# Kernel optimization log

Hardware: AMD Instinct MI355X
Metric: run time of the kernel (lower is better)

The kernel has to match this reference:

```python
import jax, jax.numpy as jnp
import numpy as np

TOP_K = 8
TEMPERATURE = 0.07
EPS = 1e-12  # matches torch F.normalize eps


def l2norm(x):
    return x / jnp.maximum(jnp.linalg.norm(x, axis=-1, keepdims=True), EPS)


def setup_inputs() -> dict:
    key = jax.random.key(0)
    k1, k2, k3, k4 = jax.random.split(key, 4)
    B, D, V, U, Q = 256, 768, 50257, 1000, 10000
    time_series_embedding = jax.random.normal(k1, (B, D), dtype=jnp.float32)
    word_embeddings = jax.random.normal(k2, (V, D), dtype=jnp.float32)
    # xavier_uniform-like init scale for the prototype parameter
    limit = float(np.sqrt(6.0 / (U + D)))
    tctp_embeddings = jax.random.uniform(k3, (U, D), dtype=jnp.float32, minval=-limit, maxval=limit)
    support_set = jax.random.normal(k4, (Q, D), dtype=jnp.float32)
    return {
        "time_series_embedding": time_series_embedding,
        "word_embeddings": word_embeddings,
        "tctp_embeddings": tctp_embeddings,
        "support_set": support_set,
    }


def reference(time_series_embedding, word_embeddings, tctp_embeddings, support_set):
    B = time_series_embedding.shape[0]

    # ---- L_proto: MSE between each word token and its nearest prototype ----
    # For unit vectors, cdist^2 = 2 - 2*cos_sim, so argmin(dist) == argmax(sim).
    w_norm = l2norm(word_embeddings)          # [V, D]
    t_norm = l2norm(tctp_embeddings)          # [U, D]
    sim_vu = jnp.einsum('vd,ud->vu', w_norm, t_norm)  # [V, U]
    nearest_idx = jnp.argmax(sim_vu, axis=1)          # [V]
    nearest_protos = t_norm[nearest_idx]              # [V, D]
    loss_proto = jnp.mean((w_norm - nearest_protos) ** 2)

    # ---- top-k nearest-neighbor TCTPs from the support set ----
    ts_norm = l2norm(time_series_embedding)   # [B, D]
    sup_norm = l2norm(support_set)            # [Q, D]
    sim_bq = jnp.einsum('bd,qd->bq', ts_norm, sup_norm)  # [B, Q]
    # smallest L2 distance == largest cosine similarity (unit vectors)
    _, topk_idx = jax.lax.top_k(sim_bq, TOP_K)           # [B, k]
    nearest_tctps = sup_norm[topk_idx]                   # [B, k, D]

    # ---- NNCL contrastive loss ----
    positive = l2norm(nearest_tctps.mean(axis=1))        # [B, D]
    pos_sim = jnp.sum(ts_norm * positive, axis=1) / TEMPERATURE   # [B]
    neg_sim = jnp.einsum('bd,cd->bc', ts_norm, ts_norm) / TEMPERATURE  # [B, B]
    neg_sim = jnp.where(jnp.eye(B, dtype=bool), -jnp.inf, neg_sim)
    logits = jnp.concatenate([pos_sim[:, None], neg_sim], axis=1)  # [B, 1+B]
    loss_nncl = -jnp.mean(jax.nn.log_softmax(logits, axis=1)[:, 0])

    return nearest_tctps, loss_proto, loss_nncl
```

## Files before the change

kernel.cpp:

```cpp
#include <hip/hip_runtime.h>
#include <hip/hip_bf16.h>
#include <math.h>

typedef __bf16 bf16_t;
typedef __bf16 bf16x8 __attribute__((ext_vector_type(8)));
typedef __bf16 bf16x4 __attribute__((ext_vector_type(4)));
typedef float  f32x4  __attribute__((ext_vector_type(4)));
typedef long   i64_t;
typedef unsigned long long u64_t;

#define D 768

__device__ inline double blk_sum(double x, double* s) {
#pragma unroll
  for (int m = 32; m; m >>= 1) x += __shfl_xor(x, m);
  __syncthreads();
  if ((threadIdx.x & 63) == 0) s[threadIdx.x >> 6] = x;
  __syncthreads();
  return s[0] + s[1] + s[2] + s[3];
}

__device__ inline double blk_max(double x, double* s) {
#pragma unroll
  for (int m = 32; m; m >>= 1) x = fmax(x, __shfl_xor(x, m));
  __syncthreads();
  if ((threadIdx.x & 63) == 0) s[threadIdx.x >> 6] = x;
  __syncthreads();
  return fmax(fmax(s[0], s[1]), fmax(s[2], s[3]));
}

__global__ __launch_bounds__(256) void norm_all(
    const float* __restrict__ Tm, const float* __restrict__ TS,
    const float* __restrict__ SUP, const float* __restrict__ Wm,
    u64_t* __restrict__ t8T, u64_t* __restrict__ w8t,
    float* __restrict__ wscale, float* __restrict__ ts_n,
    bf16_t* __restrict__ ts_bf, float* __restrict__ sup_n,
    double* __restrict__ accd,
    int U, int V, int B, int Q, int nbT, int nbTS, int nbSUP) {
  const int wave = threadIdx.x >> 6, lane = threadIdx.x & 63;
  const int bid = blockIdx.x;
  if (bid == 0 && threadIdx.x == 0) accd[0] = 0.0;

  if (bid < nbT) {
    const int row = bid * 4 + wave;
    double inv = 0.0;
    if (row < U) {
      const float4* s = (const float4*)(Tm + (size_t)row * D);
      double ss = 0.0;
#pragma unroll
      for (int j = 0; j < 3; j++) {
        float4 v = s[lane + 64 * j];
        ss += (double)v.x * v.x + (double)v.y * v.y +
              (double)v.z * v.z + (double)v.w * v.w;
      }
#pragma unroll
      for (int m = 32; m; m >>= 1) ss += __shfl_xor(ss, m);
      inv = 1.0 / fmax(sqrt(ss), 1e-12);
    }
    const float sc = (float)(inv * 16.0);
#pragma unroll
    for (int h = 0; h < 2; h++) {
      if (h == 1 && lane >= 32) continue;
      const int c = h * 64 + lane;
      u64_t frag = 0ull;
      if (row < U) {
        const float* p = Tm + (size_t)row * D + c * 8;
        float4 x = *(const float4*)p;
        float4 y = *(const float4*)(p + 4);
        int lo = __builtin_amdgcn_cvt_pk_fp8_f32(x.x * sc, x.y * sc, 0, false);
        lo = __builtin_amdgcn_cvt_pk_fp8_f32(x.z * sc, x.w * sc, lo, true);
        int hi = __builtin_amdgcn_cvt_pk_fp8_f32(y.x * sc, y.y * sc, 0, false);
        hi = __builtin_amdgcn_cvt_pk_fp8_f32(y.z * sc, y.w * sc, hi, true);
        frag = ((u64_t)(unsigned)hi << 32) | (unsigned)lo;
      }
      t8T[(size_t)c * 1024 + row] = frag;
    }
    return;
  }

  if (bid < nbT + nbTS + nbSUP) {
    const float* src;
    int row;
    bool is_ts = false;
    if (bid < nbT + nbTS) { row = (bid - nbT) * 4 + wave; src = TS; is_ts = true; }
    else                  { row = (bid - nbT - nbTS) * 4 + wave; src = SUP;
                            if (row >= Q) return; }
    const float4* s = (const float4*)(src + (size_t)row * D);
    float4 v[3];
    double ss = 0.0;
#pragma unroll
    for (int j = 0; j < 3; j++) {
      v[j] = s[lane + 64 * j];
      ss += (double)v[j].x * v[j].x + (double)v[j].y * v[j].y +
            (double)v[j].z * v[j].z + (double)v[j].w * v[j].w;
    }
#pragma unroll
    for (int m = 32; m; m >>= 1) ss += __shfl_xor(ss, m);
    double inv = 1.0 / fmax(sqrt(ss), 1e-12);
    float4 o[3];
#pragma unroll
    for (int j = 0; j < 3; j++) {
      o[j].x = (float)((double)v[j].x * inv);
      o[j].y = (float)((double)v[j].y * inv);
      o[j].z = (float)((double)v[j].z * inv);
      o[j].w = (float)((double)v[j].w * inv);
    }
    float* dst = is_ts ? ts_n : sup_n;
    float* drow = dst + (size_t)row * D;
#pragma unroll
    for (int j = 0; j < 3; j++) ((float4*)drow)[lane + 64 * j] = o[j];
    if (is_ts) {
      bf16_t* brow = ts_bf + (size_t)row * D;
#pragma unroll
      for (int j = 0; j < 3; j++) {
        bf16x4 ob;
        ob[0] = (bf16_t)o[j].x; ob[1] = (bf16_t)o[j].y;
        ob[2] = (bf16_t)o[j].z; ob[3] = (bf16_t)o[j].w;
        *(bf16x4*)(brow + 4 * (lane + 64 * j)) = ob;
      }
    }
    return;
  }

  {
    const int v0 = (bid - nbT - nbTS - nbSUP) * 64 + wave * 16;
    const int r  = lane & 15;
    const int cs = lane >> 4;
    const int v  = v0 + r;
    const bool valid = v < V;
    const float* Wp = Wm + (size_t)v * D;
    u64_t* tile = w8t + (size_t)(v0 >> 4) * 1536;
    float ssf = 0.f;
#pragma unroll
    for (int j = 0; j < 24; j++) {
      u64_t frag = 0ull;
      if (valid) {
        const float* p = Wp + (j * 4 + cs) * 8;
        float4 x = *(const float4*)p;
        float4 y = *(const float4*)(p + 4);
        ssf += x.x * x.x + x.y * x.y + x.z * x.z + x.w * x.w +
               y.x * y.x + y.y * y.y + y.z * y.z + y.w * y.w;
        int lo = __builtin_amdgcn_cvt_pk_fp8_f32(x.x * 16.f, x.y * 16.f, 0, false);
        lo = __builtin_amdgcn_cvt_pk_fp8_f32(x.z * 16.f, x.w * 16.f, lo, true);
        int hi = __builtin_amdgcn_cvt_pk_fp8_f32(y.x * 16.f, y.y * 16.f, 0, false);
        hi = __builtin_amdgcn_cvt_pk_fp8_f32(y.z * 16.f, y.w * 16.f, hi, true);
        frag = ((u64_t)(unsigned)hi << 32) | (unsigned)lo;
      }
      tile[j * 64 + lane] = frag;
    }
    ssf += __shfl_xor(ssf, 16);
    ssf += __shfl_xor(ssf, 32);
    if (cs == 0)
      wscale[v0 + r] = valid
          ? (float)(1.0 / (256.0 * fmax(sqrt((double)ssf), 1e-12)))
          : 0.f;
  }
}

__global__ __launch_bounds__(256) void maxsim_gemm(
    const u64_t* __restrict__ W8T, const u64_t* __restrict__ T8T,
    float* __restrict__ maxpart, int U, int vstride) {
  __shared__ u64_t bt[4 * 96 * 16];
  const int tid  = threadIdx.x;
  const int lane = tid & 63;
  const int r    = lane & 15;
  const int ks   = lane >> 4;
  const int g    = blockIdx.x;

  {
    const int pb = g * 64;
#pragma unroll
    for (int j = 0; j < 12; j++) {
      const int m = j * 256 + tid;
      const int s = m / 768;
      const int rem = m - s * 768;
      const int c = rem >> 3, h = rem & 7;
      ulonglong2 val = *(const ulonglong2*)(T8T + (size_t)c * 1024 + pb + s * 16 + h * 2);
      *(ulonglong2*)(bt + s * 1536 + c * 16 + h * 2) = val;
    }
  }
  __syncthreads();

  bool msk[4];
#pragma unroll
  for (int s = 0; s < 4; s++) msk[s] = (g * 64 + s * 16 + r) < U;

  const int wv = tid >> 6;
#pragma unroll
  for (int wt = 0; wt < 4; wt++) {
    const int v0 = blockIdx.y * 256 + wv * 64 + wt * 16;
    const u64_t* ap = W8T + (size_t)(v0 >> 4) * 1536;
    u64_t a[24];
#pragma unroll
    for (int kk = 0; kk < 24; kk++) a[kk] = ap[kk * 64 + lane];
    f32x4 ac0 = {0.f,0.f,0.f,0.f}, ac1 = {0.f,0.f,0.f,0.f};
    f32x4 ac2 = {0.f,0.f,0.f,0.f}, ac3 = {0.f,0.f,0.f,0.f};
#pragma unroll
    for (int kk = 0; kk < 24; kk++) {
      const int ci = kk * 64 + lane;
      ac0 = __builtin_amdgcn_mfma_f32_16x16x32_fp8_fp8(
          (i64_t)a[kk], (i64_t)bt[ci],            ac0, 0, 0, 0);
      ac1 = __builtin_amdgcn_mfma_f32_16x16x32_fp8_fp8(
          (i64_t)a[kk], (i64_t)bt[1536 + ci],     ac1, 0, 0, 0);
      ac2 = __builtin_amdgcn_mfma_f32_16x16x32_fp8_fp8(
          (i64_t)a[kk], (i64_t)bt[2 * 1536 + ci], ac2, 0, 0, 0);
      ac3 = __builtin_amdgcn_mfma_f32_16x16x32_fp8_fp8(
          (i64_t)a[kk], (i64_t)bt[3 * 1536 + ci], ac3, 0, 0, 0);
    }
    f32x4 mx = {-1e30f, -1e30f, -1e30f, -1e30f};
#pragma unroll
    for (int j = 0; j < 4; j++) {
      if (msk[0]) mx[j] = fmaxf(mx[j], ac0[j]);
      if (msk[1]) mx[j] = fmaxf(mx[j], ac1[j]);
      if (msk[2]) mx[j] = fmaxf(mx[j], ac2[j]);
      if (msk[3]) mx[j] = fmaxf(mx[j], ac3[j]);
    }
#pragma unroll
    for (int m = 1; m < 16; m <<= 1) {
#pragma unroll
      for (int j = 0; j < 4; j++) mx[j] = fmaxf(mx[j], __shfl_xor(mx[j], m));
    }
    if (r == 0) {
#pragma unroll
      for (int j = 0; j < 4; j++)
        maxpart[(size_t)g * vstride + v0 + ks * 4 + j] = mx[j];
    }
  }
}

#define LDSROW 776

__global__ __launch_bounds__(256) void simf_gemm(const float* __restrict__ SUPn,
                                                 const bf16_t* __restrict__ TSb,
                                                 float* __restrict__ sim,
                                                 int Q, int ld, int NTB) {
  __shared__ __align__(16) bf16_t lds[2][16 * LDSROW];
  const int tid  = threadIdx.x;
  const int lane = tid & 63;
  const int rowbase = blockIdx.x * 64 + (tid >> 6) * 16;
  const int arow_i  = rowbase + (lane & 15);

  bf16x8 a[24];
  if (arow_i < Q) {
    const float* ar = SUPn + (size_t)arow_i * D + ((lane >> 4) * 8);
#pragma unroll
    for (int kk = 0; kk < 24; kk++) {
      float4 x = *(const float4*)(ar + kk * 32);
      float4 y = *(const float4*)(ar + kk * 32 + 4);
      bf16x8 f;
      f[0] = (bf16_t)x.x; f[1] = (bf16_t)x.y; f[2] = (bf16_t)x.z; f[3] = (bf16_t)x.w;
      f[4] = (bf16_t)y.x; f[5] = (bf16_t)y.y; f[6] = (bf16_t)y.z; f[7] = (bf16_t)y.w;
      a[kk] = f;
    }
  } else {
#pragma unroll
    for (int kk = 0; kk < 24; kk++) {
      bf16x8 f;
#pragma unroll
      for (int e = 0; e < 8; e++) f[e] = (bf16_t)0.f;
      a[kk] = f;
    }
  }

  auto stage = [&](int buf, int nt) {
    const ulonglong2* src = (const ulonglong2*)(TSb + (size_t)nt * 16 * D);
#pragma unroll
    for (int j = 0; j < 6; j++) {
      int c = tid + j * 256;
      int rr = c / 96, w = c % 96;
      *(ulonglong2*)&lds[buf][rr * LDSROW + w * 8] = src[c];
    }
  };

  stage(0, 0);
  for (int nt = 0; nt < NTB; nt++) {
    __syncthreads();
    if (nt + 1 < NTB) stage((nt + 1) & 1, nt + 1);
    f32x4 acc = {0.f, 0.f, 0.f, 0.f};
    const bf16_t* brow = &lds[nt & 1][(lane & 15) * LDSROW + ((lane >> 4) * 8)];
#pragma unroll
    for (int kk = 0; kk < 24; kk++) {
      bf16x8 b = *(const bf16x8*)(brow + kk * 32);
      acc = __builtin_amdgcn_mfma_f32_16x16x32_bf16(a[kk], b, acc, 0, 0, 0);
    }
    const int bcol = nt * 16 + (lane & 15);
    const int q0   = rowbase + ((lane >> 4) << 2);
    float* dst = sim + (size_t)bcol * ld + q0;
    if (q0 + 3 < Q) {
      *(f32x4*)dst = acc;
    } else {
#pragma unroll
      for (int j = 0; j < 4; j++)
        if (q0 + j < Q) dst[j] = acc[j];
    }
  }
}

__global__ __launch_bounds__(256) void gram_gemm(const float* __restrict__ TSn,
                                                 float* __restrict__ gram, int Bn) {
  __shared__ float As[16][68];
  __shared__ float Bs[16][68];
  const int tid = threadIdx.x;
  const int tx = tid & 15, ty = tid >> 4;
  const int m0 = blockIdx.y * 64, n0 = blockIdx.x * 64;
  const int sr = tid >> 2, sk = (tid & 3) * 4;
  float acc[4][4] = {};
  for (int k0 = 0; k0 < D; k0 += 16) {
    __syncthreads();
    float4 av = *(const float4*)(TSn + (size_t)(m0 + sr) * D + k0 + sk);
    float4 bv = *(const float4*)(TSn + (size_t)(n0 + sr) * D + k0 + sk);
    As[sk + 0][sr] = av.x; As[sk + 1][sr] = av.y;
    As[sk + 2][sr] = av.z; As[sk + 3][sr] = av.w;
    Bs[sk + 0][sr] = bv.x; Bs[sk + 1][sr] = bv.y;
    Bs[sk + 2][sr] = bv.z; Bs[sk + 3][sr] = bv.w;
    __syncthreads();
#pragma unroll
    for (int k = 0; k < 16; k++) {
      float a0 = As[k][ty * 4 + 0], a1 = As[k][ty * 4 + 1];
      float a2 = As[k][ty * 4 + 2], a3 = As[k][ty * 4 + 3];
      float b0 = Bs[k][tx * 4 + 0], b1 = Bs[k][tx * 4 + 1];
      float b2 = Bs[k][tx * 4 + 2], b3 = Bs[k][tx * 4 + 3];
      acc[0][0] += a0 * b0; acc[0][1] += a0 * b1; acc[0][2] += a0 * b2; acc[0][3] += a0 * b3;
      acc[1][0] += a1 * b0; acc[1][1] += a1 * b1; acc[1][2] += a1 * b2; acc[1][3] += a1 * b3;
      acc[2][0] += a2 * b0; acc[2][1] += a2 * b1; acc[2][2] += a2 * b2; acc[2][3] += a2 * b3;
      acc[3][0] += a3 * b0; acc[3][1] += a3 * b1; acc[3][2] += a3 * b2; acc[3][3] += a3 * b3;
    }
  }
#pragma unroll
  for (int i = 0; i < 4; i++) {
    float4 o = {acc[i][0], acc[i][1], acc[i][2], acc[i][3]};
    *(float4*)(gram + (size_t)(m0 + ty * 4 + i) * Bn + n0 + tx * 4) = o;
  }
}

__device__ inline unsigned long long pack_key(float v, int q) {
  unsigned u = __float_as_uint(v);
  u = (u & 0x80000000u) ? ~u : (u | 0x80000000u);
  return ((unsigned long long)u << 32) | (unsigned)(0xFFFFFFFFu - (unsigned)q);
}

__global__ __launch_bounds__(256) void topk_nncl(const float* __restrict__ sim,
                                                 const float* __restrict__ gram,
                                                 const float* __restrict__ SUPn,
                                                 const float* __restrict__ TSn,
                                                 float* __restrict__ out,
                                                 double* __restrict__ row_loss,
                                                 int Q, int ld, int Bn) {
  __shared__ unsigned long long sk[256][16];
  __shared__ float tsrow[D];
  __shared__ double sval[16];
  __shared__ int    sidx[16];
  __shared__ double red[4];
  const int b = blockIdx.x, tid = threadIdx.x;
#pragma unroll
  for (int j = 0; j < 3; j++) tsrow[tid + 256 * j] = TSn[(size_t)b * D + tid + 256 * j];

  const float* row = sim + (size_t)b * ld;
  unsigned long long best[16];
#pragma unroll
  for (int k = 0; k < 16; k++) best[k] = 0ull;
  for (int q = tid; q < Q; q += 256) {
    unsigned long long key = pack_key(row[q], q);
    if (key > best[15]) {
      best[15] = key;
      for (int k = 15; k > 0; k--) {
        if (best[k] > best[k - 1]) {
          unsigned long long t = best[k]; best[k] = best[k - 1]; best[k - 1] = t;
        } else break;
      }
    }
  }
#pragma unroll
  for (int k = 0; k < 16; k++) sk[tid][k] = best[k];
  for (int stride = 128; stride >= 1; stride >>= 1) {
    __syncthreads();
    if (tid < stride) {
      unsigned long long outk[16];
      int pa = 0, pb = 0;
#pragma unroll
      for (int k = 0; k < 16; k++) {
        unsigned long long va = sk[tid][pa], vb = sk[tid + stride][pb];
        if (va >= vb) { outk[k] = va; pa++; }
        else          { outk[k] = vb; pb++; }
      }
#pragma unroll
      for (int k = 0; k < 16; k++) sk[tid][k] = outk[k];
    }
  }
  __syncthreads();

  const int lane = tid & 63, w = tid >> 6;
  for (int c = w; c < 16; c += 4) {
    int q = (int)(0xFFFFFFFFu - (unsigned)(sk[0][c] & 0xFFFFFFFFull));
    const float* sr = SUPn + (size_t)q * D;
    double dot = 0.0;
#pragma unroll
    for (int i = 0; i < 12; i++)
      dot += (double)sr[lane + 64 * i] * (double)tsrow[lane + 64 * i];
#pragma unroll
    for (int m = 32; m; m >>= 1) dot += __shfl_xor(dot, m);
    if (lane == 0) { sval[c] = dot; sidx[c] = q; }
  }
  __syncthreads();
  if (tid == 0) {
    for (int i = 1; i < 16; i++) {
      double v = sval[i]; int ix = sidx[i];
      int j = i - 1;
      while (j >= 0 && (sval[j] < v || (sval[j] == v && sidx[j] > ix))) {
        sval[j + 1] = sval[j]; sidx[j + 1] = sidx[j]; j--;
      }
      sval[j + 1] = v; sidx[j + 1] = ix;
    }
  }
  __syncthreads();

  float mean[3] = {0.f, 0.f, 0.f};
#pragma unroll
  for (int k = 0; k < 8; k++) {
    const float* sr = SUPn + (size_t)sidx[k] * D;
    float* orow = out + ((size_t)b * 8 + k) * D;
#pragma unroll
    for (int j = 0; j < 3; j++) {
      float x = sr[tid + 256 * j];
      orow[tid + 256 * j] = x;
      mean[j] += x;
    }
  }
#pragma unroll
  for (int j = 0; j < 3; j++) mean[j] *= 0.125f;
  double ss = 0.0;
#pragma unroll
  for (int j = 0; j < 3; j++) ss += (double)mean[j] * mean[j];
  ss = blk_sum(ss, red);
  double inv = 1.0 / fmax(sqrt(ss), 1e-12);
  double dot = 0.0;
#pragma unroll
  for (int j = 0; j < 3; j++)
    dot += (double)tsrow[tid + 256 * j] * ((double)mean[j] * inv);
  dot = blk_sum(dot, red);
  const double p = dot / (double)0.07f;

  const bool diag = (tid == b);
  double logit = (double)gram[(size_t)b * Bn + tid] / (double)0.07f;
  double m = blk_max(diag ? -1e300 : logit, red);
  m = fmax(m, p);
  double term = diag ? 0.0 : exp(logit - m);
  double ssum = blk_sum(term, red);
  ssum += exp(p - m);
  if (tid == 0) row_loss[b] = (log(ssum) + m) - p;
}

__global__ __launch_bounds__(256) void reduce_proto(
    const float* __restrict__ maxpart, const float* __restrict__ wscale,
    double* __restrict__ accd, int V, int vstride) {
  __shared__ double red[4];
  const int v = blockIdx.x * 256 + threadIdx.x;
  double s = 0.0;
  if (v < V) {
    float mx = -1e30f;
#pragma unroll
    for (int g = 0; g < 16; g++)
      mx = fmaxf(mx, maxpart[(size_t)g * vstride + v]);
    s = 2.0 - 2.0 * (double)mx * (double)wscale[v];
  }
  s = blk_sum(s, red);
  if (threadIdx.x == 0) atomicAdd(accd, s);
}

__global__ __launch_bounds__(256) void finalize(const double* __restrict__ accd,
                                                const double* __restrict__ row_loss,
                                                float* __restrict__ d_out, int out_size,
                                                int V, int B) {
  __shared__ double red[4];
  const int tid = threadIdx.x;
  double s2 = 0.0;
  for (int b = tid; b < B; b += 256) s2 += row_loss[b];
  s2 = blk_sum(s2, red);
  if (tid == 0) {
    d_out[out_size - 2] = (float)(accd[0] / ((double)V * (double)D));
    d_out[out_size - 1] = (float)(s2 / (double)B);
  }
}

extern "C" void kernel_launch(void* const* d_in, const int* in_sizes, int n_in,
                              void* d_out, int out_size, void* d_ws, size_t ws_size,
                              hipStream_t stream) {
  const float* TS  = (const float*)d_in[0];
  const float* W   = (const float*)d_in[1];
  const float* T   = (const float*)d_in[2];
  const float* SUP = (const float*)d_in[3];
  const int B = in_sizes[0] / D;
  const int V = in_sizes[1] / D;
  const int U = in_sizes[2] / D;
  const int Q = in_sizes[3] / D;
  const int VPAD = (V + 255) & ~255;
  const int QPAD = (Q + 63) & ~63;
  const int NTB  = B / 16;
  const int nbT  = 1024 / 4;
  const int nbTS = B / 4;
  const int nbSUP = (Q + 3) / 4;
  const int nbW  = VPAD / 64;

  char* ws = (char*)d_ws;
  size_t off = 0;
  auto alloc = [&](size_t bytes) -> char* {
    char* p = ws + off;
    off = (off + bytes + 255) & ~(size_t)255;
    return p;
  };
  u64_t*  t8T    = (u64_t*) alloc((size_t)96 * 1024 * 8);
  u64_t*  w8t    = (u64_t*) alloc((size_t)(VPAD / 16) * 1536 * 8);
  float*  wscale = (float*) alloc((size_t)VPAD * 4);
  float*  maxpart= (float*) alloc((size_t)16 * VPAD * 4);
  float*  ts_n   = (float*) alloc((size_t)B * D * 4);
  bf16_t* ts_bf  = (bf16_t*)alloc((size_t)B * D * 2);
  float*  sup_n  = (float*) alloc((size_t)Q * D * 4);
  float*  simf   = (float*) alloc((size_t)B * QPAD * 4);
  float*  gram   = (float*) alloc((size_t)B * B * 4);
  double* rloss  = (double*)alloc((size_t)B * 8);
  double* accd   = (double*)alloc(8);
  (void)ws_size; (void)n_in;

  norm_all<<<nbT + nbTS + nbSUP + nbW, 256, 0, stream>>>(
      T, TS, SUP, W, t8T, w8t, wscale, ts_n, ts_bf, sup_n, accd,
      U, V, B, Q, nbT, nbTS, nbSUP);

  dim3 gms(16, VPAD / 256);
  maxsim_gemm<<<gms, 256, 0, stream>>>(w8t, t8T, maxpart, U, VPAD);

  simf_gemm<<<QPAD / 64, 256, 0, stream>>>(sup_n, ts_bf, simf, Q, QPAD, NTB);

  dim3 ggr(B / 64, B / 64);
  gram_gemm<<<ggr, 256, 0, stream>>>(ts_n, gram, B);

  topk_nncl<<<B, 256, 0, stream>>>(simf, gram, sup_n, ts_n, (float*)d_out,
                                   rloss, Q, QPAD, B);
  reduce_proto<<<VPAD / 256, 256, 0, stream>>>(maxpart, wscale, accd, V, VPAD);
  finalize<<<1, 256, 0, stream>>>(accd, rloss, (float*)d_out, out_size, V, B);
}
```

Measured before the change: 238.7 us.

## Split top-k selection into parallel per-chunk partial kernels plus merge

The per-row top-k scan over the support-set similarities is split into 8 chunks, each handled by its own block that writes 16 candidate keys to workspace. The NNCL kernel then merges the 8 sorted candidate lists serially in one thread before the rescoring step. This targets the low parallelism of one 256-thread block per row doing a long serial insertion scan plus shared-memory merge tree. It costs an extra kernel launch, a small workspace buffer, and a serial merge step.

```diff
diff --git a/kernel.cpp b/kernel.cpp
--- a/kernel.cpp
+++ b/kernel.cpp
@@ -339,27 +339,18 @@
   return ((unsigned long long)u << 32) | (unsigned)(0xFFFFFFFFu - (unsigned)q);
 }
 
-__global__ __launch_bounds__(256) void topk_nncl(const float* __restrict__ sim,
-                                                 const float* __restrict__ gram,
-                                                 const float* __restrict__ SUPn,
-                                                 const float* __restrict__ TSn,
-                                                 float* __restrict__ out,
-                                                 double* __restrict__ row_loss,
-                                                 int Q, int ld, int Bn) {
+__global__ __launch_bounds__(256) void topk_part(const float* __restrict__ sim,
+                                                 u64_t* __restrict__ cand_keys,
+                                                 int Q, int ld, int qc) {
   __shared__ unsigned long long sk[256][16];
-  __shared__ float tsrow[D];
-  __shared__ double sval[16];
-  __shared__ int    sidx[16];
-  __shared__ double red[4];
-  const int b = blockIdx.x, tid = threadIdx.x;
-#pragma unroll
-  for (int j = 0; j < 3; j++) tsrow[tid + 256 * j] = TSn[(size_t)b * D + tid + 256 * j];
-
+  const int b = blockIdx.y, chunk = blockIdx.x, tid = threadIdx.x;
   const float* row = sim + (size_t)b * ld;
+  const int q0 = chunk * qc;
+  const int q1 = min(Q, q0 + qc);
   unsigned long long best[16];
 #pragma unroll
   for (int k = 0; k < 16; k++) best[k] = 0ull;
-  for (int q = tid; q < Q; q += 256) {
+  for (int q = q0 + tid; q < q1; q += 256) {
     unsigned long long key = pack_key(row[q], q);
     if (key > best[15]) {
       best[15] = key;
@@ -388,10 +379,45 @@
     }
   }
   __syncthreads();
+  if (tid < 16) cand_keys[((size_t)b * 8 + chunk) * 16 + tid] = sk[0][tid];
+}
+
+__global__ __launch_bounds__(256) void topk_nncl(const u64_t* __restrict__ cand_keys,
+                                                 const float* __restrict__ gram,
+                                                 const float* __restrict__ SUPn,
+                                                 const float* __restrict__ TSn,
+                                                 float* __restrict__ out,
+                                                 double* __restrict__ row_loss,
+                                                 int Bn) {
+  __shared__ u64_t keys[128];
+  __shared__ u64_t merged[16];
+  __shared__ float tsrow[D];
+  __shared__ double sval[16];
+  __shared__ int    sidx[16];
+  __shared__ double red[4];
+  const int b = blockIdx.x, tid = threadIdx.x;
+#pragma unroll
+  for (int j = 0; j < 3; j++) tsrow[tid + 256 * j] = TSn[(size_t)b * D + tid + 256 * j];
+  if (tid < 128) keys[tid] = cand_keys[(size_t)b * 128 + tid];
+  __syncthreads();
+  if (tid == 0) {
+    int p[8] = {0, 0, 0, 0, 0, 0, 0, 0};
+    for (int k = 0; k < 16; k++) {
+      u64_t bestv = 0ull; int bi = 0;
+#pragma unroll
+      for (int c = 0; c < 8; c++) {
+        u64_t v = (p[c] < 16) ? keys[c * 16 + p[c]] : 0ull;
+        if (v > bestv) { bestv = v; bi = c; }
+      }
+      merged[k] = bestv;
+      p[bi]++;
+    }
+  }
+  __syncthreads();
 
   const int lane = tid & 63, w = tid >> 6;
   for (int c = w; c < 16; c += 4) {
-    int q = (int)(0xFFFFFFFFu - (unsigned)(sk[0][c] & 0xFFFFFFFFull));
+    int q = (int)(0xFFFFFFFFu - (unsigned)(merged[c] & 0xFFFFFFFFull));
     const float* sr = SUPn + (size_t)q * D;
     double dot = 0.0;
 #pragma unroll
@@ -500,6 +526,7 @@
   const int nbTS = B / 4;
   const int nbSUP = (Q + 3) / 4;
   const int nbW  = VPAD / 64;
+  const int QC   = QPAD / 8;
 
   char* ws = (char*)d_ws;
   size_t off = 0;
@@ -517,6 +544,7 @@
   float*  sup_n  = (float*) alloc((size_t)Q * D * 4);
   float*  simf   = (float*) alloc((size_t)B * QPAD * 4);
   float*  gram   = (float*) alloc((size_t)B * B * 4);
+  u64_t*  ckeys  = (u64_t*) alloc((size_t)B * 128 * 8);
   double* rloss  = (double*)alloc((size_t)B * 8);
   double* accd   = (double*)alloc(8);
   (void)ws_size; (void)n_in;
@@ -533,8 +561,10 @@
   dim3 ggr(B / 64, B / 64);
   gram_gemm<<<ggr, 256, 0, stream>>>(ts_n, gram, B);
 
-  topk_nncl<<<B, 256, 0, stream>>>(simf, gram, sup_n, ts_n, (float*)d_out,
-                                   rloss, Q, QPAD, B);
+  dim3 gtp(8, B);
+  topk_part<<<gtp, 256, 0, stream>>>(simf, ckeys, Q, QPAD, QC);
+
+  topk_nncl<<<B, 256, 0, stream>>>(ckeys, gram, sup_n, ts_n, (float*)d_out, rloss, B);
   reduce_proto<<<VPAD / 256, 256, 0, stream>>>(maxpart, wscale, accd, V, VPAD);
   finalize<<<1, 256, 0, stream>>>(accd, rloss, (float*)d_out, out_size, V, B);
 }
```

New measurement: 263.6 us. 1.1x slower.
